# Kernel tuning notes

Measured on AMD Instinct MI355X. Metric: run time of the kernel, lower is better.

The kernel has to match this reference:

```python
import jax, jax.numpy as jnp
import numpy as np

B, C, H, W = 4, 16, 512, 512
OUT = 16
HID = 64
EPS = 1e-5


def _ln(x, g, b):
    mu = x.mean(-1, keepdims=True)
    v = x.var(-1, keepdims=True)
    return (x - mu) / jnp.sqrt(v + EPS) * g + b


def setup_inputs() -> dict:
    key = jax.random.key(0)
    ks = jax.random.split(key, 8)
    HW = H * W
    d = {}
    d['input'] = jax.random.normal(ks[0], (B, C, H, W), jnp.float32)
    d['W1'] = jax.random.normal(ks[1], (HID, HW), jnp.float32) * 0.01   # Linear1 weight [64, HW]
    d['b1'] = jnp.zeros((HID,), jnp.float32)
    d['ln1_g'] = jnp.ones((HID,), jnp.float32)
    d['ln1_b'] = jnp.zeros((HID,), jnp.float32)
    d['W2'] = jax.random.normal(ks[2], (HW, HID), jnp.float32) * 0.02   # Linear2 weight [HW, 64]
    d['b2'] = jnp.zeros((HW,), jnp.float32)
    d['ln2_g'] = jnp.ones((HW,), jnp.float32)
    d['ln2_b'] = jnp.zeros((HW,), jnp.float32)
    d['cw1'] = jax.random.normal(ks[3], (1, C, 1, 1), jnp.float32) * 0.1   # 1x1 conv C->1
    d['cb1'] = jnp.zeros((1,), jnp.float32)
    d['cw3'] = jax.random.normal(ks[4], (OUT, C, 3, 3), jnp.float32) * 0.05  # 3x3 conv C->OUT
    d['cb3'] = jnp.zeros((OUT,), jnp.float32)
    d['bn_g'] = jnp.ones((OUT,), jnp.float32)
    d['bn_b'] = jnp.zeros((OUT,), jnp.float32)
    return d


def reference(input, W1, b1, ln1_g, ln1_b, W2, b2, ln2_g, ln2_b, cw1, cb1, cw3, cb3, bn_g, bn_b):
    Bq, Cq, Hq, Wq = input.shape
    HW = Hq * Wq
    m = input.reshape(Bq, Cq, HW)
    # Linear1 -> LN -> ReLU  (per-channel over flattened spatial dim)
    h = jax.nn.relu(_ln(m @ W1.T + b1, ln1_g, ln1_b))            # [B, C, 64]
    # Linear2 -> LN -> ReLU
    m2 = jax.nn.relu(_ln(h @ W2.T + b2, ln2_g, ln2_b))           # [B, C, HW]
    m2 = m2.reshape(Bq, Cq, Hq, Wq)
    # 1x1 conv C -> 1
    score = jnp.einsum('bchw,oc->bohw', m2, cw1[:, :, 0, 0]) + cb1[:, None, None]  # [B,1,H,W]
    # keep_topk: ratio 0.25, no grad
    K = HW // 4
    flat = jax.lax.stop_gradient(score.reshape(Bq, HW))
    _, idx = jax.lax.top_k(flat, K)                               # [B, K]
    mask = jnp.zeros_like(flat).at[jnp.arange(Bq)[:, None], idx].set(1.0).reshape(Bq, 1, Hq, Wq)
    # boolean-mask gather: torch selects in ascending flat-index order
    idx_s = jnp.sort(idx, axis=1)                                 # [B, K]
    g = jnp.take_along_axis(m, idx_s[:, None, :], axis=2).reshape(Bq, Cq, Hq // 2, Wq // 2)
    # out_conv: 3x3 conv -> BatchNorm (batch stats, training mode) -> ReLU
    y = jax.lax.conv_general_dilated(g, cw3, (1, 1), [(1, 1), (1, 1)],
                                     dimension_numbers=('NCHW', 'OIHW', 'NCHW'))
    y = y + cb3[:, None, None]
    mu = y.mean((0, 2, 3), keepdims=True)
    v = y.var((0, 2, 3), keepdims=True)
    y = jax.nn.relu((y - mu) / jnp.sqrt(v + EPS) * bn_g[:, None, None] + bn_b[:, None, None])
    return (y, mask)
```

## Files before the change

### kernel.cpp

```cpp
#include <hip/hip_runtime.h>

#define HWN    262144
#define KSEL   65536
#define TIECAP 2048

#define OFF_H      0
#define OFF_DOT1   32768
#define OFF_G      65536
#define OFF_WBAR   98304
#define OFF_WB     98816
#define OFF_SB     99328
#define OFF_MU2    99360
#define OFF_ISIG2  99872
#define OFF_STATE  100384
#define OFF_HIST   100448
#define OFF_TIECNT 116832
#define OFF_CHCNT  116848
#define OFF_TIELST 116864
#define OFF_CHLST  149632
#define OFF_BCNT   182400
#define OFF_BOFF   186496
#define OFF_BNP    190592
#define OFF_BNC    452736
#define OFF_PART2  458752
#define OFF_HT     1015808
#define REGION2    1048576

#define PS_GRAM 4226
#define PS_DOT  4096

typedef double d4_t __attribute__((ext_vector_type(4)));
typedef float  f4v  __attribute__((ext_vector_type(4)));

__device__ __forceinline__ unsigned monokey(double s){
  unsigned long long b = (unsigned long long)__double_as_longlong(s);
  b = (b & 0x8000000000000000ULL) ? ~b : (b | 0x8000000000000000ULL);
  return (unsigned)(b >> 32);
}

__global__ void k_zero(unsigned* hist, unsigned* tiecnt, unsigned* chcnt, unsigned* state){
  int t = threadIdx.x;
  for (int i = t; i < 4096; i += 256) hist[i] = 0u;
  if (t < 4){
    tiecnt[t] = 0u; chcnt[t] = 0u;
    state[t*4+0] = 0u;
    state[t*4+1] = (unsigned)KSEL;
    state[t*4+2] = 0u;
    state[t*4+3] = 0u;
  }
}

__device__ __forceinline__ void st_tile(double* __restrict__ P, const d4_t& acc,
                                        const int* ri_, const int* ci_, int ai, int bi){
#pragma unroll
  for (int i = 0; i < 4; i++){
    int ri = ri_[i], ci = ci_[i];
    if (bi < 4)            P[(ai*16+ri)*66 + bi*16 + ci] = acc[i];
    else if (ai < 4){ if (ci < 2) P[(ai*16+ri)*66 + 64 + ci] = acc[i]; }
    else { if (ri == 0 && ci < 2) P[4224 + ci] = acc[i]; }
  }
}

#define GRAM_STEP(F0,F1,F2,F3,FB) { \
  double f0=(double)(F0), f1=(double)(F1), f2=(double)(F2), f3=(double)(F3); \
  double f4=(m==0)?(double)(FB):((m==1)?1.0:0.0); \
  if (w == 0){ \
    accA = __builtin_amdgcn_mfma_f64_16x16x4f64(f0, f0, accA, 0, 0, 0); \
    accB = __builtin_amdgcn_mfma_f64_16x16x4f64(f0, f1, accB, 0, 0, 0); \
    accC = __builtin_amdgcn_mfma_f64_16x16x4f64(f0, f2, accC, 0, 0, 0); \
    accD = __builtin_amdgcn_mfma_f64_16x16x4f64(f0, f3, accD, 0, 0, 0); \
  } else if (w == 1){ \
    accA = __builtin_amdgcn_mfma_f64_16x16x4f64(f1, f1, accA, 0, 0, 0); \
    accB = __builtin_amdgcn_mfma_f64_16x16x4f64(f1, f2, accB, 0, 0, 0); \
    accC = __builtin_amdgcn_mfma_f64_16x16x4f64(f1, f3, accC, 0, 0, 0); \
    accD = __builtin_amdgcn_mfma_f64_16x16x4f64(f1, f4, accD, 0, 0, 0); \
  } else if (w == 2){ \
    accA = __builtin_amdgcn_mfma_f64_16x16x4f64(f2, f2, accA, 0, 0, 0); \
    accB = __builtin_amdgcn_mfma_f64_16x16x4f64(f2, f3, accB, 0, 0, 0); \
    accC = __builtin_amdgcn_mfma_f64_16x16x4f64(f2, f4, accC, 0, 0, 0); \
    accD = __builtin_amdgcn_mfma_f64_16x16x4f64(f3, f4, accD, 0, 0, 0); \
  } else { \
    accA = __builtin_amdgcn_mfma_f64_16x16x4f64(f3, f3, accA, 0, 0, 0); \
    accB = __builtin_amdgcn_mfma_f64_16x16x4f64(f0, f4, accB, 0, 0, 0); \
    accC = __builtin_amdgcn_mfma_f64_16x16x4f64(f4, f4, accC, 0, 0, 0); \
  } }

#define G1_STEP(AV,B0,B1,B2,B3) { \
  _Pragma("unroll") \
  for (int t4 = 0; t4 < 4; t4++){ \
    double a = (double)(AV)[t4]; \
    acc0 = __builtin_amdgcn_mfma_f64_16x16x4f64(a, (double)(B0)[t4], acc0, 0, 0, 0); \
    acc1 = __builtin_amdgcn_mfma_f64_16x16x4f64(a, (double)(B1)[t4], acc1, 0, 0, 0); \
    acc2 = __builtin_amdgcn_mfma_f64_16x16x4f64(a, (double)(B2)[t4], acc2, 0, 0, 0); \
    acc3 = __builtin_amdgcn_mfma_f64_16x16x4f64(a, (double)(B3)[t4], acc3, 0, 0, 0); \
  } }

__global__ __launch_bounds__(256) void k_mm(const float* __restrict__ W2,
                                            const float* __restrict__ b2,
                                            const float* __restrict__ inp,
                                            const float* __restrict__ W1,
                                            double* __restrict__ partG,
                                            double* __restrict__ partD,
                                            int pPerBlk, int NBH){
  int t = threadIdx.x;
  int w = t >> 6, l = t & 63;
  int q = l >> 4, m = l & 15;
  if ((int)blockIdx.x < NBH){
    int p0 = blockIdx.x * pPerBlk;
    d4_t accA = {0.,0.,0.,0.}, accB = {0.,0.,0.,0.};
    d4_t accC = {0.,0.,0.,0.}, accD = {0.,0.,0.,0.};
    const float* base = W2 + (size_t)(p0 + q)*64 + m;
    const float* b2p  = b2 + p0 + q;
    int nPair = pPerBlk >> 3;
    float gA0 = base[0], gA1 = base[16], gA2 = base[32], gA3 = base[48];
    float gAb = b2p[0];
    for (int i = 0; i < nPair; i++){
      float gB0 = base[256+0], gB1 = base[256+16], gB2 = base[256+32], gB3 = base[256+48];
      float gBb = b2p[4];
      GRAM_STEP(gA0, gA1, gA2, gA3, gAb)
      base += 512; b2p += 8;
      if (i + 1 < nPair){
        gA0 = base[0]; gA1 = base[16]; gA2 = base[32]; gA3 = base[48];
        gAb = b2p[0];
      }
      GRAM_STEP(gB0, gB1, gB2, gB3, gBb)
    }
    d4_t prD = {0.,0.,0.,0.}, pcD = {0.,0.,0.,0.};
    double rp = (double)(1 + m);
    prD = __builtin_amdgcn_mfma_f64_16x16x4f64(rp, 1.0, prD, 0, 0, 0);
    pcD = __builtin_amdgcn_mfma_f64_16x16x4f64(1.0, rp, pcD, 0, 0, 0);
    int ri_[4], ci_[4];
#pragma unroll
    for (int i = 0; i < 4; i++){
      ri_[i] = ((((int)prD[i]) >> 2) - 1) & 15;
      ci_[i] = ((((int)pcD[i]) >> 2) - 1) & 15;
    }
    double* P = partG + (size_t)blockIdx.x * PS_GRAM;
    if (w == 0){
      st_tile(P, accA, ri_, ci_, 0, 0); st_tile(P, accB, ri_, ci_, 0, 1);
      st_tile(P, accC, ri_, ci_, 0, 2); st_tile(P, accD, ri_, ci_, 0, 3);
    } else if (w == 1){
      st_tile(P, accA, ri_, ci_, 1, 1); st_tile(P, accB, ri_, ci_, 1, 2);
      st_tile(P, accC, ri_, ci_, 1, 3); st_tile(P, accD, ri_, ci_, 1, 4);
    } else if (w == 2){
      st_tile(P, accA, ri_, ci_, 2, 2); st_tile(P, accB, ri_, ci_, 2, 3);
      st_tile(P, accC, ri_, ci_, 2, 4); st_tile(P, accD, ri_, ci_, 3, 4);
    } else {
      st_tile(P, accA, ri_, ci_, 3, 3); st_tile(P, accB, ri_, ci_, 0, 4);
      st_tile(P, accC, ri_, ci_, 4, 4);
    }
  } else {
    int blk = (int)blockIdx.x - NBH;
    int p0 = blk * pPerBlk;
    d4_t acc0 = {0.,0.,0.,0.}, acc1 = {0.,0.,0.,0.};
    d4_t acc2 = {0.,0.,0.,0.}, acc3 = {0.,0.,0.,0.};
    const f4v* ap  = (const f4v*)(inp + (size_t)(w*16 + m)*HWN + p0 + q*4);
    const f4v* bp0 = (const f4v*)(W1  + (size_t)( 0 + m)*HWN + p0 + q*4);
    const f4v* bp1 = (const f4v*)(W1  + (size_t)(16 + m)*HWN + p0 + q*4);
    const f4v* bp2 = (const f4v*)(W1  + (size_t)(32 + m)*HWN + p0 + q*4);
    const f4v* bp3 = (const f4v*)(W1  + (size_t)(48 + m)*HWN + p0 + q*4);
    int nPair = pPerBlk >> 5;
    f4v avA = ap[0], b0A = bp0[0], b1A = bp1[0], b2A = bp2[0], b3A = bp3[0];
    for (int i = 0; i < nPair; i++){
      size_t x1 = (size_t)(2*i+1)*4;
      f4v avB = ap[x1], b0B = bp0[x1], b1B = bp1[x1], b2B = bp2[x1], b3B = bp3[x1];
      G1_STEP(avA, b0A, b1A, b2A, b3A)
      if (i + 1 < nPair){
        size_t x2 = (size_t)(2*i+2)*4;
        avA = ap[x2]; b0A = bp0[x2]; b1A = bp1[x2]; b2A = bp2[x2]; b3A = bp3[x2];
      }
      G1_STEP(avB, b0B, b1B, b2B, b3B)
    }
    d4_t prD = {0.,0.,0.,0.}, pcD = {0.,0.,0.,0.};
    double rp = (double)(1 + m);
    prD = __builtin_amdgcn_mfma_f64_16x16x4f64(rp, 1.0, prD, 0, 0, 0);
    pcD = __builtin_amdgcn_mfma_f64_16x16x4f64(1.0, rp, pcD, 0, 0, 0);
    double* P = partD + (size_t)blk * PS_DOT;
#pragma unroll
    for (int i = 0; i < 4; i++){
      int ri = ((((int)prD[i]) >> 2) - 1) & 15;
      int ci = ((((int)pcD[i]) >> 2) - 1) & 15;
      int r = w*16 + ri;
      P[r*64 +  0 + ci] = acc0[i];
      P[r*64 + 16 + ci] = acc1[i];
      P[r*64 + 32 + ci] = acc2[i];
      P[r*64 + 48 + ci] = acc3[i];
    }
  }
}

__global__ __launch_bounds__(256) void k_red1(const double* __restrict__ part,
                                              double* __restrict__ part2,
                                              int bPerGrp, int cnt){
  int nj = (cnt + 255) >> 8;
  int jc = blockIdx.x % nj;
  int grp = blockIdx.x / nj;
  int j = jc*256 + threadIdx.x;
  if (j >= cnt) return;
  const double* p = part + (size_t)grp * bPerGrp * cnt + j;
  double s0=0.0, s1=0.0, s2=0.0, s3=0.0;
  for (int b = 0; b < bPerGrp; b += 4){
    s0 += p[(size_t)(b+0)*cnt];
    s1 += p[(size_t)(b+1)*cnt];
    s2 += p[(size_t)(b+2)*cnt];
    s3 += p[(size_t)(b+3)*cnt];
  }
  part2[(size_t)grp*cnt + j] = (s0+s1) + (s2+s3);
}

__global__ void k_redgram2(const double* __restrict__ part2,
                           double* __restrict__ G, double* __restrict__ wb,
                           double* __restrict__ wbar, double* __restrict__ sbv){
  int j = blockIdx.x*256 + threadIdx.x;
  if (j >= PS_GRAM) return;
  int src = j;
  int r = 0, c = 0;
  if (j < 4224){
    r = j / 66; c = j % 66;
    if (c < 64){
      int rb = r >> 4, cb = c >> 4;
      if (cb < rb)
        src = ((cb*16 + (c & 15)) * 66) + rb*16 + (r & 15);
    }
  }
  double s = 0.0;
#pragma unroll
  for (int b = 0; b < 16; b++) s += part2[(size_t)b*PS_GRAM + src];
  if (j < 4224){
    if (c < 64) G[r*64 + c] = s;
    else if (c == 64) wb[r] = s;
    else wbar[r] = s;
  } else if (j == 4224) sbv[1] = s;
  else sbv[0] = s;
}

__global__ void k_reddot2(const double* __restrict__ part2, double* __restrict__ dot1){
  int j = blockIdx.x*256 + threadIdx.x;
  if (j >= PS_DOT) return;
  double s = 0.0;
#pragma unroll
  for (int b = 0; b < 16; b++) s += part2[(size_t)b*PS_DOT + j];
  dot1[j] = s;
}

__global__ void k_h(const double* __restrict__ dot1, const float* __restrict__ b1,
                    const float* __restrict__ g1, const float* __restrict__ b1l,
                    const double* __restrict__ wbar, const double* __restrict__ sbv,
                    double* __restrict__ h, double* __restrict__ hT,
                    double* __restrict__ mu2){
  int r = threadIdx.x;
  double m = 0.0;
  for (int k=0;k<64;k++) m += dot1[r*64+k] + (double)b1[k];
  m *= (1.0/64.0);
  double v = 0.0;
  for (int k=0;k<64;k++){ double d = dot1[r*64+k] + (double)b1[k] - m; v += d*d; }
  v *= (1.0/64.0);
  double inv = 1.0 / sqrt(v + 1e-5);
  double s2 = 0.0;
  for (int k=0;k<64;k++){
    double x = dot1[r*64+k] + (double)b1[k];
    double z = (x - m) * inv;
    double hv = z * (double)g1[k] + (double)b1l[k];
    hv = hv > 0.0 ? hv : 0.0;
    h[r*64+k] = hv;
    hT[k*64+r] = hv;
    s2 += hv * wbar[k];
  }
  mu2[r] = (s2 + sbv[0]) / (double)HWN;
}

__global__ void k_var2(const double* __restrict__ h, const double* __restrict__ G,
                       const double* __restrict__ wb, const double* __restrict__ sbv,
                       const double* __restrict__ mu2, double* __restrict__ isig2){
  int r = blockIdx.x, k = threadIdx.x;
  double hk = h[r*64+k];
  double v = 0.0;
  for (int l=0;l<64;l++) v += G[k*64+l] * h[r*64+l];
  double contrib = hk*v + 2.0*hk*wb[k];
  for (int o=32;o>0;o>>=1) contrib += __shfl_down(contrib, o);
  if (k == 0){
    double E2 = (contrib + sbv[1]) / (double)HWN;
    double mu = mu2[r];
    double var = E2 - mu*mu;
    isig2[r] = 1.0 / sqrt(var + 1e-5);
  }
}

#define SC_K(WF, KIDX) { \
  double w_ = (double)(WF); \
  const double* hp_ = hb + (KIDX)*64; \
  acc[0]+=hp_[0]*w_;  acc[1]+=hp_[1]*w_;  acc[2]+=hp_[2]*w_;  acc[3]+=hp_[3]*w_; \
  acc[4]+=hp_[4]*w_;  acc[5]+=hp_[5]*w_;  acc[6]+=hp_[6]*w_;  acc[7]+=hp_[7]*w_; \
  acc[8]+=hp_[8]*w_;  acc[9]+=hp_[9]*w_;  acc[10]+=hp_[10]*w_; acc[11]+=hp_[11]*w_; \
  acc[12]+=hp_[12]*w_; acc[13]+=hp_[13]*w_; acc[14]+=hp_[14]*w_; acc[15]+=hp_[15]*w_; }

__global__ __launch_bounds__(256) void k_score(const float* __restrict__ W2,
    const float* __restrict__ b2, const float* __restrict__ g2, const float* __restrict__ lb2,
    const float* __restrict__ cw1, const float* __restrict__ cb1,
    const double* __restrict__ hT, const double* __restrict__ mu2, const double* __restrict__ isg,
    double* __restrict__ score, unsigned* __restrict__ key){
  int t = threadIdx.x;
  int p = blockIdx.x*256 + t;
  float4 w4[16];
  const float4* wp = (const float4*)(W2 + (size_t)p*64);
#pragma unroll
  for (int i=0;i<16;i++) w4[i] = wp[i];
  double g2p = (double)g2[p], lb2p = (double)lb2[p], b2p = (double)b2[p];
  double cb = (double)cb1[0];
  for (int b = 0; b < 4; b++){
    double acc[16];
#pragma unroll
    for (int j=0;j<16;j++) acc[j]=0.0;
    const double* hb = hT + b*16;
#pragma unroll
    for (int k4=0;k4<16;k4++){
      float4 wv = w4[k4];
      SC_K(wv.x, (k4*4+0))
      SC_K(wv.y, (k4*4+1))
      SC_K(wv.z, (k4*4+2))
      SC_K(wv.w, (k4*4+3))
    }
    double sc = cb;
#pragma unroll
    for (int j=0;j<16;j++){
      int c = b*16 + j;
      double tv = acc[j] + b2p;
      double z = (tv - mu2[c]) * isg[c];
      double v = z * g2p + lb2p;
      v = v > 0.0 ? v : 0.0;
      sc += v * (double)cw1[j];
    }
    if (sc == 0.0) sc = 0.0;
    score[(size_t)b*HWN + p] = sc;
    key[(size_t)b*HWN + p] = monokey(sc);
  }
}

__global__ void k_hist(const unsigned* __restrict__ key, const unsigned* __restrict__ state,
                       unsigned* __restrict__ hist, int pass){
  __shared__ unsigned lh[256];
  int t = threadIdx.x;
  int b = blockIdx.x >> 7, seg = blockIdx.x & 127;
  lh[t] = 0u;
  __syncthreads();
  unsigned pref = state[b*4+0];
  const unsigned* kb = key + (size_t)b*HWN + seg*2048;
  int shb = 24 - 8*pass;
#pragma unroll
  for (int i=0;i<8;i++){
    unsigned kk = kb[t + 256*i];
    bool ok = (pass == 0) || ((kk >> (32 - 8*pass)) == pref);
    if (ok) atomicAdd(&lh[(kk >> shb) & 255u], 1u);
  }
  __syncthreads();
  atomicAdd(&hist[(pass*4 + b)*256 + t], lh[t]);
}

__global__ void k_scan(unsigned* __restrict__ state, const unsigned* __restrict__ hist, int pass){
  __shared__ unsigned ls[4*256];
  int t = threadIdx.x;
  int b = t >> 8, j = t & 255;
  unsigned cnt = hist[(pass*4 + b)*256 + j];
  int q = 255 - j;
  ls[b*256 + q] = cnt;
  __syncthreads();
  for (int o=1;o<256;o<<=1){
    unsigned v = (q >= o) ? ls[b*256 + q - o] : 0u;
    __syncthreads();
    ls[b*256 + q] += v;
    __syncthreads();
  }
  unsigned need = state[b*4+1];
  unsigned pref = state[b*4+0];
  unsigned GT = (j == 255) ? 0u : ls[b*256 + (254 - j)];
  unsigned GE = ls[b*256 + (255 - j)];
  if (GT < need && need <= GE){
    unsigned npref = (pref << 8) | (unsigned)j;
    state[b*4+0] = npref;
    state[b*4+1] = need - GT;
    if (pass == 3){ state[b*4+2] = npref; state[b*4+3] = need - GT; }
  }
}

__global__ __launch_bounds__(256) void k_mask(const unsigned* __restrict__ key,
    const unsigned* __restrict__ state, float* __restrict__ outM,
    unsigned* __restrict__ bcnt, unsigned* __restrict__ tiecnt, unsigned* __restrict__ tielist){
  __shared__ int red[256];
  int t = threadIdx.x;
  int b = blockIdx.x >> 8, seg = blockIdx.x & 255;
  unsigned T = state[b*4+2];
  int p0 = seg*1024 + t*4;
  size_t base = (size_t)b*HWN + p0;
  uint4 kk = *((const uint4*)(key + base));
  float4 mv; int cnt = 0;
  { int s = kk.x > T; mv.x = s ? 1.f : 0.f; cnt += s;
    if (kk.x == T){ unsigned ti = atomicAdd(&tiecnt[b],1u); if (ti < TIECAP) tielist[b*TIECAP+ti] = (unsigned)(p0+0); } }
  { int s = kk.y > T; mv.y = s ? 1.f : 0.f; cnt += s;
    if (kk.y == T){ unsigned ti = atomicAdd(&tiecnt[b],1u); if (ti < TIECAP) tielist[b*TIECAP+ti] = (unsigned)(p0+1); } }
  { int s = kk.z > T; mv.z = s ? 1.f : 0.f; cnt += s;
    if (kk.z == T){ unsigned ti = atomicAdd(&tiecnt[b],1u); if (ti < TIECAP) tielist[b*TIECAP+ti] = (unsigned)(p0+2); } }
  { int s = kk.w > T; mv.w = s ? 1.f : 0.f; cnt += s;
    if (kk.w == T){ unsigned ti = atomicAdd(&tiecnt[b],1u); if (ti < TIECAP) tielist[b*TIECAP+ti] = (unsigned)(p0+3); } }
  *((float4*)(outM + base)) = mv;
  red[t] = cnt;
  __syncthreads();
  for (int o=128;o>0;o>>=1){ if (t < o) red[t] += red[t+o]; __syncthreads(); }
  if (t == 0) bcnt[b*256 + seg] = (unsigned)red[0];
}

__global__ __launch_bounds__(256) void k_ties(const unsigned* __restrict__ state,
    const unsigned* __restrict__ tiecnt, const unsigned* __restrict__ tielist,
    const double* __restrict__ score, float* __restrict__ outM,
    unsigned* __restrict__ chcnt, unsigned* __restrict__ chlist){
  __shared__ double ssc[TIECAP];
  __shared__ unsigned spp[TIECAP];
  __shared__ unsigned skeep[TIECAP];
  int b = blockIdx.x, t = threadIdx.x;
  unsigned tc = tiecnt[b];
  int n = (int)(tc < (unsigned)TIECAP ? tc : (unsigned)TIECAP);
  unsigned nt = state[b*4+3];
  for (int i=t;i<n;i+=256){
    unsigned p = tielist[b*TIECAP+i];
    spp[i] = p; ssc[i] = score[(size_t)b*HWN + p];
  }
  __syncthreads();
  for (int i=t;i<n;i+=256){
    double si = ssc[i]; unsigned pi = spp[i]; int r = 0;
    for (int j=0;j<n;j++){
      double sj = ssc[j]; unsigned pj = spp[j];
      if (sj > si || (sj == si && pj < pi)) r++;
    }
    skeep[i] = (r < (int)nt) ? 1u : 0u;
  }
  __syncthreads();
  for (int i=t;i<n;i+=256){
    if (skeep[i]){
      unsigned pi = spp[i]; int r2 = 0;
      for (int j=0;j<n;j++) if (skeep[j] && spp[j] < pi) r2++;
      chlist[b*TIECAP + r2] = pi;
      outM[(size_t)b*HWN + pi] = 1.0f;
    }
  }
  if (t == 0){
    unsigned c = ((unsigned)n < nt) ? (unsigned)n : nt;
    chcnt[b] = c;
  }
}

__global__ void k_scanblk(const unsigned* __restrict__ bcnt, unsigned* __restrict__ boff){
  __shared__ unsigned ls[1024];
  int t = threadIdx.x; int b = t >> 8, j = t & 255;
  unsigned own = bcnt[b*256 + j];
  ls[t] = own;
  __syncthreads();
  for (int o=1;o<256;o<<=1){
    unsigned v = (j >= o) ? ls[b*256 + j - o] : 0u;
    __syncthreads();
    ls[t] += v;
    __syncthreads();
  }
  boff[b*256 + j] = ls[t] - own;
}

__device__ __forceinline__ void gath_one(unsigned kv, int p, unsigned T,
    const unsigned* __restrict__ cl, unsigned nch, unsigned base, int& run,
    const float* __restrict__ inp, float* __restrict__ g, int b){
  int isGT = kv > T;
  int isCh = 0;
  if (kv == T && nch > 0u){
    for (unsigned j=0;j<nch;j++) if (cl[j] == (unsigned)p){ isCh = 1; break; }
  }
  if (isGT | isCh){
    unsigned adj = 0;
    for (unsigned j=0;j<nch;j++) adj += (cl[j] < (unsigned)p) ? 1u : 0u;
    unsigned rank = base + (unsigned)run + adj;
#pragma unroll
    for (int c=0;c<16;c++)
      g[(size_t)(b*16+c)*KSEL + rank] = inp[(size_t)(b*16+c)*HWN + p];
  }
  run += isGT;
}

__global__ __launch_bounds__(256) void k_gather(const unsigned* __restrict__ key,
    const unsigned* __restrict__ state, const unsigned* __restrict__ boff,
    const unsigned* __restrict__ chcnt, const unsigned* __restrict__ chlist,
    const float* __restrict__ inp, float* __restrict__ g){
  __shared__ int wt[4];
  int t = threadIdx.x;
  int b = blockIdx.x >> 8, seg = blockIdx.x & 255;
  unsigned T = state[b*4+2];
  int p0 = seg*1024 + t*4;
  uint4 kk = *((const uint4*)(key + (size_t)b*HWN + p0));
  int s0 = kk.x > T, s1 = kk.y > T, s2 = kk.z > T, s3 = kk.w > T;
  int cnt = s0 + s1 + s2 + s3;
  int l = t & 63;
  int incl = cnt;
#pragma unroll
  for (int o=1;o<64;o<<=1){ int v = __shfl_up(incl, o); if (l >= o) incl += v; }
  int w = t >> 6;
  if (l == 63) wt[w] = incl;
  __syncthreads();
  int wex = 0;
#pragma unroll
  for (int i=0;i<4;i++) if (i < w) wex += wt[i];
  int exth = incl - cnt;
  unsigned base = boff[b*256 + seg] + (unsigned)wex + (unsigned)exth;
  unsigned nch = chcnt[b];
  const unsigned* cl = chlist + b*TIECAP;
  int run = 0;
  gath_one(kk.x, p0+0, T, cl, nch, base, run, inp, g, b);
  gath_one(kk.y, p0+1, T, cl, nch, base, run, inp, g, b);
  gath_one(kk.z, p0+2, T, cl, nch, base, run, inp, g, b);
  gath_one(kk.w, p0+3, T, cl, nch, base, run, inp, g, b);
}

__global__ __launch_bounds__(256) void k_conv(const float* __restrict__ g,
    const float* __restrict__ cw3, const float* __restrict__ cb3,
    float* __restrict__ outY, double* __restrict__ bnp){
  __shared__ float wsm[2304];
  __shared__ float it[18*18];
  __shared__ double red[16][4][2];
  int t = threadIdx.x;
  int b = blockIdx.x >> 8, tile = blockIdx.x & 255;
  int ty0 = (tile >> 4) * 16, tx0 = (tile & 15) * 16;
  int tx = t & 15, ty = t >> 4;
#pragma unroll
  for (int i=0;i<9;i++){ int j = t + 256*i; if (j < 2304) wsm[j] = cw3[j]; }
  float acc[16];
#pragma unroll
  for (int i=0;i<16;i++) acc[i] = 0.f;
  for (int ic=0; ic<16; ic++){
    __syncthreads();
    for (int j=t;j<324;j+=256){
      int gy = ty0 - 1 + j/18, gx = tx0 - 1 + (j%18);
      float v = 0.f;
      if (gy >= 0 && gy < 256 && gx >= 0 && gx < 256)
        v = g[(size_t)(b*16+ic)*KSEL + gy*256 + gx];
      it[j] = v;
    }
    __syncthreads();
#pragma unroll
    for (int ky=0;ky<3;ky++)
#pragma unroll
      for (int kx=0;kx<3;kx++){
        float v = it[(ty+ky)*18 + tx+kx];
#pragma unroll
        for (int oc=0;oc<16;oc++) acc[oc] += v * wsm[oc*144 + ic*9 + ky*3 + kx];
      }
  }
  int w = t >> 6, l = t & 63;
  for (int oc=0;oc<16;oc++){
    float yv = acc[oc] + cb3[oc];
    outY[(size_t)(b*16+oc)*KSEL + (ty0+ty)*256 + tx0+tx] = yv;
    double s = (double)yv, q = (double)yv*(double)yv;
    for (int o=32;o>0;o>>=1){ s += __shfl_down(s, o); q += __shfl_down(q, o); }
    if (l == 0){ red[oc][w][0] = s; red[oc][w][1] = q; }
  }
  __syncthreads();
  if (t < 16){
    double s=0.0, q=0.0;
    for (int w2=0;w2<4;w2++){ s += red[t][w2][0]; q += red[t][w2][1]; }
    bnp[(size_t)blockIdx.x*32 + t*2]   = s;
    bnp[(size_t)blockIdx.x*32 + t*2+1] = q;
  }
}

__global__ void k_bnred(const double* __restrict__ bnp, const float* __restrict__ bng,
                        const float* __restrict__ bnb, float* __restrict__ bnc){
  __shared__ double red[16][16][2];
  int t = threadIdx.x; int oc = t >> 4, sl = t & 15;
  double s = 0.0, q = 0.0;
  for (int i=0;i<64;i++){
    int blk = sl*64 + i;
    s += bnp[(size_t)blk*32 + oc*2];
    q += bnp[(size_t)blk*32 + oc*2+1];
  }
  red[oc][sl][0] = s; red[oc][sl][1] = q;
  __syncthreads();
  if (t < 16){
    double S=0.0, Q=0.0;
    for (int i=0;i<16;i++){ S += red[t][i][0]; Q += red[t][i][1]; }
    double N = 262144.0;
    double mu = S/N, var = Q/N - mu*mu;
    double inv = 1.0 / sqrt(var + 1e-5);
    double a = (double)bng[t] * inv;
    double bsh = (double)bnb[t] - mu*a;
    bnc[t*2] = (float)a; bnc[t*2+1] = (float)bsh;
  }
}

__global__ void k_bnapply(float* __restrict__ outY, const float* __restrict__ bnc){
  int i = blockIdx.x*256 + threadIdx.x;
  float4 v = ((float4*)outY)[i];
  int oc = (i >> 14) & 15;
  float a = bnc[oc*2], bsh = bnc[oc*2+1];
  v.x = fmaxf(v.x*a + bsh, 0.f);
  v.y = fmaxf(v.y*a + bsh, 0.f);
  v.z = fmaxf(v.z*a + bsh, 0.f);
  v.w = fmaxf(v.w*a + bsh, 0.f);
  ((float4*)outY)[i] = v;
}

extern "C" void kernel_launch(void* const* d_in, const int* in_sizes, int n_in,
                              void* d_out, int out_size, void* d_ws, size_t ws_size,
                              hipStream_t stream){
  const float* inp  = (const float*)d_in[0];
  const float* W1   = (const float*)d_in[1];
  const float* b1   = (const float*)d_in[2];
  const float* g1   = (const float*)d_in[3];
  const float* b1l  = (const float*)d_in[4];
  const float* W2   = (const float*)d_in[5];
  const float* b2   = (const float*)d_in[6];
  const float* g2   = (const float*)d_in[7];
  const float* lb2  = (const float*)d_in[8];
  const float* cw1  = (const float*)d_in[9];
  const float* cb1  = (const float*)d_in[10];
  const float* cw3  = (const float*)d_in[11];
  const float* cb3  = (const float*)d_in[12];
  const float* bng  = (const float*)d_in[13];
  const float* bnb  = (const float*)d_in[14];
  (void)in_sizes; (void)n_in; (void)out_size;

  char* ws = (char*)d_ws;
  float* outY = (float*)d_out;
  float* outM = outY + 4194304;

  size_t need512  = (size_t)REGION2 + 512ull*4352*8 + 16777216ull;
  int NBH = (ws_size >= need512) ? 512 : 128;
  int pPerBlk = HWN / NBH;
  int bPerGrp = NBH / 16;

  double*  partG  = (double*)(ws + REGION2);
  double*  partD  = (double*)(ws + REGION2 + (size_t)NBH*PS_GRAM*8);
  double*  score  = (double*)(ws + REGION2);
  unsigned* key   = (unsigned*)(ws + REGION2 + 8388608ull);
  float*   gbuf   = (float*)(ws + REGION2 + 12582912ull);
  double*  hbuf   = (double*)(ws + OFF_H);
  double*  hTbuf  = (double*)(ws + OFF_HT);
  double*  dot1   = (double*)(ws + OFF_DOT1);
  double*  G      = (double*)(ws + OFF_G);
  double*  wbar   = (double*)(ws + OFF_WBAR);
  double*  wb     = (double*)(ws + OFF_WB);
  double*  sbv    = (double*)(ws + OFF_SB);
  double*  mu2    = (double*)(ws + OFF_MU2);
  double*  isg    = (double*)(ws + OFF_ISIG2);
  unsigned* state = (unsigned*)(ws + OFF_STATE);
  unsigned* hist  = (unsigned*)(ws + OFF_HIST);
  unsigned* tiecnt= (unsigned*)(ws + OFF_TIECNT);
  unsigned* chcnt = (unsigned*)(ws + OFF_CHCNT);
  unsigned* tielist=(unsigned*)(ws + OFF_TIELST);
  unsigned* chlist= (unsigned*)(ws + OFF_CHLST);
  unsigned* bcnt  = (unsigned*)(ws + OFF_BCNT);
  unsigned* boff  = (unsigned*)(ws + OFF_BOFF);
  double*  bnp    = (double*)(ws + OFF_BNP);
  float*   bnc    = (float*)(ws + OFF_BNC);
  double*  part2  = (double*)(ws + OFF_PART2);

  k_zero<<<1, 256, 0, stream>>>(hist, tiecnt, chcnt, state);
  k_mm<<<2*NBH, 256, 0, stream>>>(W2, b2, inp, W1, partG, partD, pPerBlk, NBH);
  k_red1<<<17*16, 256, 0, stream>>>(partG, part2, bPerGrp, PS_GRAM);
  k_redgram2<<<17, 256, 0, stream>>>(part2, G, wb, wbar, sbv);
  k_red1<<<16*16, 256, 0, stream>>>(partD, part2, bPerGrp, PS_DOT);
  k_reddot2<<<16, 256, 0, stream>>>(part2, dot1);
  k_h<<<1, 64, 0, stream>>>(dot1, b1, g1, b1l, wbar, sbv, hbuf, hTbuf, mu2);
  k_var2<<<64, 64, 0, stream>>>(hbuf, G, wb, sbv, mu2, isg);
  k_score<<<1024, 256, 0, stream>>>(W2, b2, g2, lb2, cw1, cb1, hTbuf, mu2, isg, score, key);
  for (int pass = 0; pass < 4; pass++){
    k_hist<<<512, 256, 0, stream>>>(key, state, hist, pass);
    k_scan<<<1, 1024, 0, stream>>>(state, hist, pass);
  }
  k_mask<<<1024, 256, 0, stream>>>(key, state, outM, bcnt, tiecnt, tielist);
  k_ties<<<4, 256, 0, stream>>>(state, tiecnt, tielist, score, outM, chcnt, chlist);
  k_scanblk<<<1, 1024, 0, stream>>>(bcnt, boff);
  k_gather<<<1024, 256, 0, stream>>>(key, state, boff, chcnt, chlist, inp, gbuf);
  k_conv<<<1024, 256, 0, stream>>>(gbuf, cw3, cb3, outY, bnp);
  k_bnred<<<1, 256, 0, stream>>>(bnp, bng, bnb, bnc);
  k_bnapply<<<4096, 256, 0, stream>>>(outY, bnc);
}
```

Baseline: 378.5 us.

## Compute bias/mean Gram terms with scalar sums and fuse first radix histogram into scoring

```diff
diff --git a/kernel.cpp b/kernel.cpp
--- a/kernel.cpp
+++ b/kernel.cpp
@@ -53,36 +53,30 @@
 __device__ __forceinline__ void st_tile(double* __restrict__ P, const d4_t& acc,
                                         const int* ri_, const int* ci_, int ai, int bi){
 #pragma unroll
-  for (int i = 0; i < 4; i++){
-    int ri = ri_[i], ci = ci_[i];
-    if (bi < 4)            P[(ai*16+ri)*66 + bi*16 + ci] = acc[i];
-    else if (ai < 4){ if (ci < 2) P[(ai*16+ri)*66 + 64 + ci] = acc[i]; }
-    else { if (ri == 0 && ci < 2) P[4224 + ci] = acc[i]; }
-  }
+  for (int i = 0; i < 4; i++)
+    P[(ai*16+ri_[i])*66 + bi*16 + ci_[i]] = acc[i];
 }
 
 #define GRAM_STEP(F0,F1,F2,F3,FB) { \
   double f0=(double)(F0), f1=(double)(F1), f2=(double)(F2), f3=(double)(F3); \
-  double f4=(m==0)?(double)(FB):((m==1)?1.0:0.0); \
   if (w == 0){ \
     accA = __builtin_amdgcn_mfma_f64_16x16x4f64(f0, f0, accA, 0, 0, 0); \
     accB = __builtin_amdgcn_mfma_f64_16x16x4f64(f0, f1, accB, 0, 0, 0); \
     accC = __builtin_amdgcn_mfma_f64_16x16x4f64(f0, f2, accC, 0, 0, 0); \
-    accD = __builtin_amdgcn_mfma_f64_16x16x4f64(f0, f3, accD, 0, 0, 0); \
   } else if (w == 1){ \
-    accA = __builtin_amdgcn_mfma_f64_16x16x4f64(f1, f1, accA, 0, 0, 0); \
-    accB = __builtin_amdgcn_mfma_f64_16x16x4f64(f1, f2, accB, 0, 0, 0); \
-    accC = __builtin_amdgcn_mfma_f64_16x16x4f64(f1, f3, accC, 0, 0, 0); \
-    accD = __builtin_amdgcn_mfma_f64_16x16x4f64(f1, f4, accD, 0, 0, 0); \
+    accA = __builtin_amdgcn_mfma_f64_16x16x4f64(f0, f3, accA, 0, 0, 0); \
+    accB = __builtin_amdgcn_mfma_f64_16x16x4f64(f1, f1, accB, 0, 0, 0); \
+    accC = __builtin_amdgcn_mfma_f64_16x16x4f64(f1, f2, accC, 0, 0, 0); \
   } else if (w == 2){ \
-    accA = __builtin_amdgcn_mfma_f64_16x16x4f64(f2, f2, accA, 0, 0, 0); \
-    accB = __builtin_amdgcn_mfma_f64_16x16x4f64(f2, f3, accB, 0, 0, 0); \
-    accC = __builtin_amdgcn_mfma_f64_16x16x4f64(f2, f4, accC, 0, 0, 0); \
-    accD = __builtin_amdgcn_mfma_f64_16x16x4f64(f3, f4, accD, 0, 0, 0); \
+    accA = __builtin_amdgcn_mfma_f64_16x16x4f64(f1, f3, accA, 0, 0, 0); \
+    accB = __builtin_amdgcn_mfma_f64_16x16x4f64(f2, f2, accB, 0, 0, 0); \
+    accC = __builtin_amdgcn_mfma_f64_16x16x4f64(f2, f3, accC, 0, 0, 0); \
   } else { \
     accA = __builtin_amdgcn_mfma_f64_16x16x4f64(f3, f3, accA, 0, 0, 0); \
-    accB = __builtin_amdgcn_mfma_f64_16x16x4f64(f0, f4, accB, 0, 0, 0); \
-    accC = __builtin_amdgcn_mfma_f64_16x16x4f64(f4, f4, accC, 0, 0, 0); \
+    double bb = (double)(FB); \
+    wbar0 += f0; wbar1 += f1; wbar2 += f2; wbar3 += f3; \
+    wb0 += f0*bb; wb1 += f1*bb; wb2 += f2*bb; wb3 += f3*bb; \
+    sb += bb; sb2 += bb*bb; \
   } }
 
 #define G1_STEP(AV,B0,B1,B2,B3) { \
@@ -107,8 +101,9 @@
   int q = l >> 4, m = l & 15;
   if ((int)blockIdx.x < NBH){
     int p0 = blockIdx.x * pPerBlk;
-    d4_t accA = {0.,0.,0.,0.}, accB = {0.,0.,0.,0.};
-    d4_t accC = {0.,0.,0.,0.}, accD = {0.,0.,0.,0.};
+    d4_t accA = {0.,0.,0.,0.}, accB = {0.,0.,0.,0.}, accC = {0.,0.,0.,0.};
+    double wbar0=0., wbar1=0., wbar2=0., wbar3=0.;
+    double wb0=0., wb1=0., wb2=0., wb3=0., sb=0., sb2=0.;
     const float* base = W2 + (size_t)(p0 + q)*64 + m;
     const float* b2p  = b2 + p0 + q;
     int nPair = pPerBlk >> 3;
@@ -138,16 +133,32 @@
     double* P = partG + (size_t)blockIdx.x * PS_GRAM;
     if (w == 0){
       st_tile(P, accA, ri_, ci_, 0, 0); st_tile(P, accB, ri_, ci_, 0, 1);
-      st_tile(P, accC, ri_, ci_, 0, 2); st_tile(P, accD, ri_, ci_, 0, 3);
+      st_tile(P, accC, ri_, ci_, 0, 2);
     } else if (w == 1){
-      st_tile(P, accA, ri_, ci_, 1, 1); st_tile(P, accB, ri_, ci_, 1, 2);
-      st_tile(P, accC, ri_, ci_, 1, 3); st_tile(P, accD, ri_, ci_, 1, 4);
+      st_tile(P, accA, ri_, ci_, 0, 3); st_tile(P, accB, ri_, ci_, 1, 1);
+      st_tile(P, accC, ri_, ci_, 1, 2);
     } else if (w == 2){
-      st_tile(P, accA, ri_, ci_, 2, 2); st_tile(P, accB, ri_, ci_, 2, 3);
-      st_tile(P, accC, ri_, ci_, 2, 4); st_tile(P, accD, ri_, ci_, 3, 4);
+      st_tile(P, accA, ri_, ci_, 1, 3); st_tile(P, accB, ri_, ci_, 2, 2);
+      st_tile(P, accC, ri_, ci_, 2, 3);
     } else {
-      st_tile(P, accA, ri_, ci_, 3, 3); st_tile(P, accB, ri_, ci_, 0, 4);
-      st_tile(P, accC, ri_, ci_, 4, 4);
+      st_tile(P, accA, ri_, ci_, 3, 3);
+      wbar0 += __shfl_down(wbar0, 32); wbar1 += __shfl_down(wbar1, 32);
+      wbar2 += __shfl_down(wbar2, 32); wbar3 += __shfl_down(wbar3, 32);
+      wb0 += __shfl_down(wb0, 32); wb1 += __shfl_down(wb1, 32);
+      wb2 += __shfl_down(wb2, 32); wb3 += __shfl_down(wb3, 32);
+      sb += __shfl_down(sb, 32); sb2 += __shfl_down(sb2, 32);
+      wbar0 += __shfl_down(wbar0, 16); wbar1 += __shfl_down(wbar1, 16);
+      wbar2 += __shfl_down(wbar2, 16); wbar3 += __shfl_down(wbar3, 16);
+      wb0 += __shfl_down(wb0, 16); wb1 += __shfl_down(wb1, 16);
+      wb2 += __shfl_down(wb2, 16); wb3 += __shfl_down(wb3, 16);
+      sb += __shfl_down(sb, 16); sb2 += __shfl_down(sb2, 16);
+      if (l < 16){
+        P[(m +  0)*66 + 64] = wb0;  P[(m +  0)*66 + 65] = wbar0;
+        P[(m + 16)*66 + 64] = wb1;  P[(m + 16)*66 + 65] = wbar1;
+        P[(m + 32)*66 + 64] = wb2;  P[(m + 32)*66 + 65] = wbar2;
+        P[(m + 48)*66 + 64] = wb3;  P[(m + 48)*66 + 65] = wbar3;
+      }
+      if (l == 0){ P[4224] = sb2; P[4225] = sb; }
     }
   } else {
     int blk = (int)blockIdx.x - NBH;
@@ -298,8 +309,11 @@
     const float* __restrict__ b2, const float* __restrict__ g2, const float* __restrict__ lb2,
     const float* __restrict__ cw1, const float* __restrict__ cb1,
     const double* __restrict__ hT, const double* __restrict__ mu2, const double* __restrict__ isg,
-    double* __restrict__ score, unsigned* __restrict__ key){
+    double* __restrict__ score, unsigned* __restrict__ key, unsigned* __restrict__ hist){
+  __shared__ unsigned lh[1024];
   int t = threadIdx.x;
+  for (int i = t; i < 1024; i += 256) lh[i] = 0u;
+  __syncthreads();
   int p = blockIdx.x*256 + t;
   float4 w4[16];
   const float4* wp = (const float4*)(W2 + (size_t)p*64);
@@ -331,9 +345,15 @@
       sc += v * (double)cw1[j];
     }
     if (sc == 0.0) sc = 0.0;
+    unsigned kk = monokey(sc);
     score[(size_t)b*HWN + p] = sc;
-    key[(size_t)b*HWN + p] = monokey(sc);
-  }
+    key[(size_t)b*HWN + p] = kk;
+    atomicAdd(&lh[b*256 + (kk >> 24)], 1u);
+  }
+  __syncthreads();
+#pragma unroll
+  for (int b = 0; b < 4; b++)
+    atomicAdd(&hist[b*256 + t], lh[b*256 + t]);
 }
 
 __global__ void k_hist(const unsigned* __restrict__ key, const unsigned* __restrict__ state,
@@ -664,8 +684,9 @@
   k_reddot2<<<16, 256, 0, stream>>>(part2, dot1);
   k_h<<<1, 64, 0, stream>>>(dot1, b1, g1, b1l, wbar, sbv, hbuf, hTbuf, mu2);
   k_var2<<<64, 64, 0, stream>>>(hbuf, G, wb, sbv, mu2, isg);
-  k_score<<<1024, 256, 0, stream>>>(W2, b2, g2, lb2, cw1, cb1, hTbuf, mu2, isg, score, key);
-  for (int pass = 0; pass < 4; pass++){
+  k_score<<<1024, 256, 0, stream>>>(W2, b2, g2, lb2, cw1, cb1, hTbuf, mu2, isg, score, key, hist);
+  k_scan<<<1, 1024, 0, stream>>>(state, hist, 0);
+  for (int pass = 1; pass < 4; pass++){
     k_hist<<<512, 256, 0, stream>>>(key, state, hist, pass);
     k_scan<<<1, 1024, 0, stream>>>(state, hist, pass);
   }
```

Measured after the change: 387.3 us. 1.02x slower.
